# Performance work log

Hardware: AMD Instinct MI355X
Metric: run time of the kernel (lower is better)

Reference implementation:

```python
import jax, jax.numpy as jnp
import numpy as np

G, HQ, D = 8, 4, 64        # kv groups, query heads per group, head size
S, HID = 2048, 2048        # tokens (single prefill sequence), hidden size
SCALE = D ** -0.5


def _rope(x, cos, sin):
    # x: [S, ..., D]; cos/sin: [S, D//2]; GPT-NeoX rotate-half style
    half = D // 2
    shape = (S,) + (1,) * (x.ndim - 2) + (half,)
    c = cos.reshape(shape)
    s = sin.reshape(shape)
    x1, x2 = x[..., :half], x[..., half:]
    return jnp.concatenate([x1 * c - x2 * s, x2 * c + x1 * s], axis=-1)


def setup_inputs() -> dict:
    key = jax.random.key(0)
    k1, k2, k3 = jax.random.split(key, 3)
    hidden_states = jax.random.normal(k1, (S, HID), dtype=jnp.float32)
    w_qkv = jax.random.normal(k2, (HID, G * (HQ + 2) * D), dtype=jnp.float32) * 0.02
    w_dense = jax.random.normal(k3, (HID, HID), dtype=jnp.float32) * 0.02
    inv_freq = 1.0 / (10000.0 ** (jnp.arange(0, D, 2, dtype=jnp.float32) / D))
    freqs = jnp.arange(S, dtype=jnp.float32)[:, None] * inv_freq[None, :]  # [S, D//2]
    return {"hidden_states": hidden_states, "cos": jnp.cos(freqs), "sin": jnp.sin(freqs),
            "w_qkv": w_qkv, "w_dense": w_dense}


def reference(hidden_states, cos, sin, w_qkv, w_dense):
    qkv = hidden_states @ w_qkv                       # [S, G*(HQ+2)*D]
    qkv = qkv.reshape(S, G, HQ + 2, D)
    q = qkv[:, :, :HQ]                                # [S, G, HQ, D]
    k = qkv[:, :, HQ]                                 # [S, G, D]
    v = qkv[:, :, HQ + 1]                             # [S, G, D]
    q = _rope(q, cos, sin)
    k = _rope(k, cos, sin)
    # causal GQA attention (prefill path, single sequence)
    scores = jnp.einsum('sghd,tgd->ghst', q, k) * SCALE   # [G, HQ, S, S]
    causal = jnp.tril(jnp.ones((S, S), dtype=bool))
    scores = jnp.where(causal, scores, jnp.float32(-1e30))
    attn = jax.nn.softmax(scores, axis=-1)
    out = jnp.einsum('ghst,tgd->sghd', attn, v)           # [S, G, HQ, D]
    return out.reshape(S, G * HQ * D) @ w_dense
```

## Files before the change

### kernel.cpp

```cpp
#include <hip/hip_runtime.h>

#define S_LEN 2048
#define HID_DIM 2048
#define NG 8
#define NHQ 4
#define DH 64
#define QSCALE 0.18033688011112042f
#define FIXMAX 12.0f

typedef short short8 __attribute__((ext_vector_type(8)));
typedef float f32x4 __attribute__((ext_vector_type(4)));
typedef unsigned short ushort_t;

__device__ __forceinline__ unsigned short f2bf(float f) {
  unsigned u = __builtin_bit_cast(unsigned, f);
  u += 0x7fffu + ((u >> 16) & 1u);
  return (unsigned short)(u >> 16);
}

__device__ __forceinline__ void mfma16(f32x4& d, short8 a, short8 b) {
  asm volatile("v_mfma_f32_16x16x32_bf16 %0, %1, %2, %0" : "+v"(d) : "v"(a), "v"(b));
}

#define GLDS16(gp, lp) __builtin_amdgcn_global_load_lds( \
    (__attribute__((address_space(1))) void*)(gp),       \
    (__attribute__((address_space(3))) void*)(lp), 16, 0, 0)

__global__ __launch_bounds__(256) void cvt_bf16_k(const float* __restrict__ in,
                                                  ushort_t* __restrict__ out, int n4) {
  int i = blockIdx.x * 256 + threadIdx.x;
  if (i >= n4) return;
  float4 v = ((const float4*)in)[i];
  ushort4 o;
  o.x = f2bf(v.x); o.y = f2bf(v.y); o.z = f2bf(v.z); o.w = f2bf(v.w);
  ((ushort4*)out)[i] = o;
}

__global__ __launch_bounds__(256) void tcvt_k(const float* __restrict__ in,
                                              ushort_t* __restrict__ out, int R, int C) {
  __shared__ ushort_t t[32][33];
  int bx = blockIdx.x * 32, by = blockIdx.y * 32;
  int tx = threadIdx.x & 31, ty = threadIdx.x >> 5;
  for (int j = ty; j < 32; j += 8)
    t[j][tx] = f2bf(in[(long)(by + j) * C + bx + tx]);
  __syncthreads();
  for (int j = ty; j < 32; j += 8)
    out[(long)(bx + j) * R + by + tx] = t[tx][j];
}

__global__ __launch_bounds__(256) void cs_trans_k(const float* __restrict__ cosb,
                                                  const float* __restrict__ sinb,
                                                  float* __restrict__ cosT,
                                                  float* __restrict__ sinT) {
  int idx = blockIdx.x * 256 + threadIdx.x;
  int s = idx >> 5, i = idx & 31;
  cosT[i * 2048 + s] = cosb[s * 32 + i];
  sinT[i * 2048 + s] = sinb[s * 32 + i];
}

#define GEMM_PROLOG()                                                       \
  const int tid = threadIdx.x;                                              \
  const int w = tid >> 6, lane = tid & 63;                                  \
  const int m0 = blockIdx.y * 128, n0 = blockIdx.x * 128;                   \
  const int sl = lane >> 3;                                                 \
  const int sc = (lane & 7) ^ sl;                                           \
  const ushort_t* Ag = A + (size_t)(m0 + 32 * w + sl) * K + sc * 8;         \
  const ushort_t* Bg = BT + (size_t)(n0 + 32 * w + sl) * K + sc * 8;        \
  f32x4 acc[4][4];                                                          \
  _Pragma("unroll") for (int i = 0; i < 4; ++i)                             \
  _Pragma("unroll") for (int j = 0; j < 4; ++j)                             \
      acc[i][j] = (f32x4){0.f, 0.f, 0.f, 0.f};                              \
  const int fr = lane & 15;                                                 \
  const int kq4 = lane >> 4;                                                \
  const int wm = w >> 1, wn = w & 1;

#define GEMM_KLOOP()                                                        \
  for (int kt = 0; kt < K; kt += 64) {                                      \
    GLDS16(Ag,          &Al[(32 * w) * 64]);                                \
    GLDS16(Ag +  8 * K, &Al[(32 * w + 8) * 64]);                            \
    GLDS16(Ag + 16 * K, &Al[(32 * w + 16) * 64]);                           \
    GLDS16(Ag + 24 * K, &Al[(32 * w + 24) * 64]);                           \
    GLDS16(Bg,          &Bl[(32 * w) * 64]);                                \
    GLDS16(Bg +  8 * K, &Bl[(32 * w + 8) * 64]);                            \
    GLDS16(Bg + 16 * K, &Bl[(32 * w + 16) * 64]);                           \
    GLDS16(Bg + 24 * K, &Bl[(32 * w + 24) * 64]);                           \
    Ag += 64; Bg += 64;                                                     \
    __syncthreads();                                                        \
    _Pragma("unroll")                                                       \
    for (int c = 0; c < 2; ++c) {                                           \
      short8 af[4], bfr[4];                                                 \
      _Pragma("unroll") for (int mf = 0; mf < 4; ++mf) {                    \
        const int row = 64 * wm + 16 * mf + fr;                             \
        af[mf] = *(const short8*)&Al[row * 64 +                             \
                 (((kq4 + 4 * c) ^ (row & 7)) << 3)];                       \
      }                                                                     \
      _Pragma("unroll") for (int nf = 0; nf < 4; ++nf) {                    \
        const int row = 64 * wn + 16 * nf + fr;                             \
        bfr[nf] = *(const short8*)&Bl[row * 64 +                            \
                  (((kq4 + 4 * c) ^ (row & 7)) << 3)];                      \
      }                                                                     \
      _Pragma("unroll") for (int mf = 0; mf < 4; ++mf)                      \
      _Pragma("unroll") for (int nf = 0; nf < 4; ++nf)                      \
          mfma16(acc[mf][nf], af[mf], bfr[nf]);                             \
    }                                                                       \
    __syncthreads();                                                        \
  }

__global__ __launch_bounds__(256) void gemm_bt_k(const ushort_t* __restrict__ A,
                                                 const ushort_t* __restrict__ BT,
                                                 float* __restrict__ C,
                                                 int M, int N, int K) {
  __shared__ __align__(16) ushort_t Al[128 * 64];
  __shared__ __align__(16) ushort_t Bl[128 * 64];
  GEMM_PROLOG();
  GEMM_KLOOP();
  const int crow = m0 + 64 * wm + 4 * (lane >> 4);
  const int ccol = n0 + 64 * wn + fr;
#pragma unroll
  for (int mf = 0; mf < 4; ++mf)
#pragma unroll
    for (int nf = 0; nf < 4; ++nf)
#pragma unroll
      for (int r = 0; r < 4; ++r)
        C[(size_t)(crow + 16 * mf + r) * N + ccol + 16 * nf] = acc[mf][nf][r];
}

__global__ __launch_bounds__(256) void gemm_qkv_k(const ushort_t* __restrict__ A,
                                                  const ushort_t* __restrict__ BT,
                                                  const float* __restrict__ cosT,
                                                  const float* __restrict__ sinT,
                                                  ushort_t* __restrict__ Qbf,
                                                  ushort_t* __restrict__ Kbf,
                                                  ushort_t* __restrict__ Vbuf,
                                                  int M, int N, int K) {
  __shared__ __align__(16) ushort_t Al[128 * 64];
  __shared__ __align__(16) ushort_t Bl[128 * 64];
  GEMM_PROLOG();
  GEMM_KLOOP();
  const int crow = m0 + 64 * wm + 4 * (lane >> 4);
  const int hb = ((n0 % 384) >> 6) + wn;
  const int gg = n0 / 384;
  if (hb == 5) {
    ushort_t* dst = Vbuf + (size_t)gg * 2048 * 64;
#pragma unroll
    for (int mf = 0; mf < 4; ++mf)
#pragma unroll
      for (int nf = 0; nf < 4; ++nf)
#pragma unroll
        for (int r = 0; r < 4; ++r)
          dst[(size_t)(crow + 16 * mf + r) * 64 + 16 * nf + fr] =
              f2bf(acc[mf][nf][r]);
  } else {
    const float qs = (hb < 4) ? QSCALE : 1.0f;
    ushort_t* dst = (hb < 4) ? Qbf + (size_t)(gg * 4 + hb) * 2048 * 64
                             : Kbf + (size_t)gg * 2048 * 64;
#pragma unroll
    for (int mf = 0; mf < 4; ++mf) {
#pragma unroll
      for (int nf2 = 0; nf2 < 2; ++nf2) {
        const int i = 16 * nf2 + fr;
        float4 cT = *(const float4*)&cosT[(size_t)i * 2048 + crow + 16 * mf];
        float4 sT = *(const float4*)&sinT[(size_t)i * 2048 + crow + 16 * mf];
        const float cc[4] = {cT.x, cT.y, cT.z, cT.w};
        const float ss[4] = {sT.x, sT.y, sT.z, sT.w};
#pragma unroll
        for (int r = 0; r < 4; ++r) {
          const size_t row = crow + 16 * mf + r;
          float x1 = acc[mf][nf2][r], x2 = acc[mf][nf2 + 2][r];
          dst[row * 64 + i]      = f2bf((x1 * cc[r] - x2 * ss[r]) * qs);
          dst[row * 64 + i + 32] = f2bf((x2 * cc[r] + x1 * ss[r]) * qs);
        }
      }
    }
  }
}

__global__ __launch_bounds__(256) void vtrans_k(const ushort_t* __restrict__ Vbuf,
                                                ushort_t* __restrict__ Vt) {
  __shared__ ushort_t t[64][65];
  int s0 = blockIdx.x * 64, g = blockIdx.y;
  for (int idx = threadIdx.x; idx < 4096; idx += 256) {
    int r = idx >> 6, d = idx & 63;
    t[d][r] = Vbuf[((size_t)g * 2048 + s0 + r) * 64 + d];
  }
  __syncthreads();
  for (int idx = threadIdx.x; idx < 4096; idx += 256) {
    int d = idx >> 6, c = idx & 63;
    Vt[((size_t)g * 64 + d) * 2048 + s0 + c] = t[d][c];
  }
}

__global__ __launch_bounds__(256, 4) void attn9_k(const ushort_t* __restrict__ Qbf,
                                                  const ushort_t* __restrict__ Kbf,
                                                  const ushort_t* __restrict__ Vt,
                                                  ushort_t* __restrict__ outb) {
  __shared__ __align__(16) ushort_t Kl[2][64 * 64];
  __shared__ __align__(16) ushort_t Vl[2][64 * 64];
  __shared__ __align__(16) ushort_t Pl[4][1024];
  const int gh = blockIdx.x;
  const int y = blockIdx.y;
  const int bb = y & 7, aa = y >> 3;
  const int u = (aa == 0) ? 31 - bb : (aa == 1) ? 16 + bb : (aa == 2) ? 15 - bb : bb;
  const int g = gh >> 2;
  const int w = threadIdx.x >> 6, l = threadIdx.x & 63;
  const int li = l & 15, hi = l >> 4;
  const int q0 = 64 * u + 16 * w;
  const int nt = u + 1;

  const ushort_t* Qh = Qbf + (long)gh * 2048 * 64;
  const ushort_t* Kh = Kbf + (long)g * 2048 * 64;
  const ushort_t* Vh = Vt + (long)g * 64 * 2048;
  char* Pw = (char*)&Pl[w][0];

  const int sr = 16 * w + (l >> 3);
  const int sc = (l & 7) ^ (l >> 3);
  const short8 ones = {0x3F80, 0x3F80, 0x3F80, 0x3F80, 0x3F80, 0x3F80, 0x3F80, 0x3F80};

  short8 aq0 = *(const short8*)&Qh[(q0 + li) * 64 + hi * 8];
  short8 aq1 = *(const short8*)&Qh[(q0 + li) * 64 + 32 + hi * 8];

  f32x4 o[4];
#pragma unroll
  for (int df = 0; df < 4; ++df) o[df] = (f32x4){0.f, 0.f, 0.f, 0.f};
  f32x4 os = (f32x4){0.f, 0.f, 0.f, 0.f};

  GLDS16(Kh + (long)sr * 64 + sc * 8,         &Kl[0][(16 * w) * 64]);
  GLDS16(Kh + (long)(sr + 8) * 64 + sc * 8,   &Kl[0][(16 * w + 8) * 64]);
  GLDS16(Vh + (long)sr * 2048 + sc * 8,       &Vl[0][(16 * w) * 64]);
  GLDS16(Vh + (long)(sr + 8) * 2048 + sc * 8, &Vl[0][(16 * w + 8) * 64]);
  __syncthreads();

  int buf = 0;
  for (int it = 0; it < nt; ++it) {
    const int t0 = it * 64;
    if (it + 1 < nt) {
      const int tn = t0 + 64;
      GLDS16(Kh + (long)(tn + sr) * 64 + sc * 8,       &Kl[buf ^ 1][(16 * w) * 64]);
      GLDS16(Kh + (long)(tn + sr + 8) * 64 + sc * 8,   &Kl[buf ^ 1][(16 * w + 8) * 64]);
      GLDS16(Vh + (long)sr * 2048 + tn + sc * 8,       &Vl[buf ^ 1][(16 * w) * 64]);
      GLDS16(Vh + (long)(sr + 8) * 2048 + tn + sc * 8, &Vl[buf ^ 1][(16 * w + 8) * 64]);
    }
    const ushort_t* kb = &Kl[buf][0];
    const ushort_t* vb = &Vl[buf][0];

    f32x4 sf[4];
#pragma unroll
    for (int f = 0; f < 4; ++f) sf[f] = (f32x4){0.f, 0.f, 0.f, 0.f};
    __builtin_amdgcn_s_setprio(1);
#pragma unroll
    for (int f = 0; f < 4; ++f) {
      const int row = 16 * f + li;
      short8 b0 = *(const short8*)&kb[row * 64 + ((hi ^ (row & 7)) << 3)];
      short8 b1 = *(const short8*)&kb[row * 64 + (((hi + 4) ^ (row & 7)) << 3)];
      mfma16(sf[f], aq0, b0);
      mfma16(sf[f], aq1, b1);
    }
    __builtin_amdgcn_s_setprio(0);

    if (t0 + 63 > q0) {
#pragma unroll
      for (int f = 0; f < 4; ++f) {
        int t = t0 + 16 * f + li;
#pragma unroll
        for (int r = 0; r < 4; ++r)
          if (t > q0 + 4 * hi + r) sf[f][r] = -1e30f;
      }
    }
#pragma unroll
    for (int f = 0; f < 4; ++f) {
      int k2 = 2 * (li + 16 * f);
#pragma unroll
      for (int r = 0; r < 4; ++r) {
        float p = __builtin_amdgcn_exp2f(sf[f][r] - FIXMAX);
        int q = 4 * hi + r;
        *(ushort_t*)(Pw + q * 128 + (k2 ^ ((q & 7) << 4))) =
            (ushort_t)(__builtin_bit_cast(unsigned, p) >> 16);
      }
    }

    __builtin_amdgcn_s_setprio(1);
#pragma unroll
    for (int kst = 0; kst < 2; ++kst) {
      short8 pa = *(const short8*)(Pw + li * 128 + (((4 * kst + hi) ^ (li & 7)) << 4));
#pragma unroll
      for (int df = 0; df < 4; ++df) {
        const int row = 16 * df + li;
        short8 bv = *(const short8*)&vb[row * 64 + (((4 * kst + hi) ^ (row & 7)) << 3)];
        mfma16(o[df], pa, bv);
      }
      mfma16(os, pa, ones);
    }
    __builtin_amdgcn_s_setprio(0);

    __syncthreads();
    buf ^= 1;
  }
#pragma unroll
  for (int r = 0; r < 4; ++r) {
    float inv = 1.f / os[r];
#pragma unroll
    for (int df = 0; df < 4; ++df)
      outb[(long)(q0 + 4 * hi + r) * HID_DIM + gh * 64 + 16 * df + li] =
          f2bf(o[df][r] * inv);
  }
}

extern "C" void kernel_launch(void* const* d_in, const int* in_sizes, int n_in,
                              void* d_out, int out_size, void* d_ws, size_t ws_size,
                              hipStream_t stream) {
  const float* X    = (const float*)d_in[0];
  const float* cosb = (const float*)d_in[1];
  const float* sinb = (const float*)d_in[2];
  const float* Wqkv = (const float*)d_in[3];
  const float* Wd   = (const float*)d_in[4];
  float* out = (float*)d_out;

  char* ws = (char*)d_ws;
  ushort_t* Xbf   = (ushort_t*)ws;
  ushort_t* WqkvT = Xbf + (size_t)2048 * 2048;
  ushort_t* WdT   = WqkvT + (size_t)3072 * 2048;
  ushort_t* Qbf   = WdT + (size_t)2048 * 2048;
  ushort_t* Kbf   = Qbf + (size_t)32 * 2048 * 64;
  ushort_t* Vbuf  = Kbf + (size_t)8 * 2048 * 64;
  ushort_t* Vt    = Vbuf + (size_t)8 * 2048 * 64;
  ushort_t* attnO = Vt + (size_t)8 * 2048 * 64;
  float*    cosT  = (float*)(attnO + (size_t)2048 * 2048);
  float*    sinT  = cosT + (size_t)32 * 2048;

  cvt_bf16_k<<<4096, 256, 0, stream>>>(X, Xbf, (2048 * 2048) / 4);
  tcvt_k<<<dim3(3072 / 32, 2048 / 32), 256, 0, stream>>>(Wqkv, WqkvT, 2048, 3072);
  tcvt_k<<<dim3(2048 / 32, 2048 / 32), 256, 0, stream>>>(Wd, WdT, 2048, 2048);
  cs_trans_k<<<256, 256, 0, stream>>>(cosb, sinb, cosT, sinT);

  gemm_qkv_k<<<dim3(3072 / 128, 2048 / 128), 256, 0, stream>>>(
      Xbf, WqkvT, cosT, sinT, Qbf, Kbf, Vbuf, 2048, 3072, 2048);

  vtrans_k<<<dim3(S_LEN / 64, NG), 256, 0, stream>>>(Vbuf, Vt);

  attn9_k<<<dim3(NG * NHQ, 32), 256, 0, stream>>>(Qbf, Kbf, Vt, attnO);

  gemm_bt_k<<<dim3(2048 / 128, 2048 / 128), 256, 0, stream>>>(attnO, WdT, out,
                                                              2048, 2048, 2048);
}
```

Before: 145.2 us.

## Enlarge attention query tile to 128 rows, two 16-row slabs per wave

Each attention block now covers 128 query rows instead of 64, with every wave handling two 16-row query slabs that share each loaded K/V tile. This halves the number of K/V tile loads from global memory per query row and reuses each LDS B-fragment read for two MFMAs. Waves skip compute on tiles that lie entirely above their causal diagonal. The cost is more registers (launch bounds lowered to 2 blocks per SIMD), a larger P buffer in LDS, half as many blocks, and some intra-block imbalance from the skipped tiles.

After: 154.9 us. 1.07x slower.

```diff
diff --git a/kernel.cpp b/kernel.cpp
--- a/kernel.cpp
+++ b/kernel.cpp
@@ -190,118 +190,143 @@
   }
 }
 
-__global__ __launch_bounds__(256, 4) void attn9_k(const ushort_t* __restrict__ Qbf,
-                                                  const ushort_t* __restrict__ Kbf,
-                                                  const ushort_t* __restrict__ Vt,
-                                                  ushort_t* __restrict__ outb) {
+__global__ __launch_bounds__(256, 2) void attn10_k(const ushort_t* __restrict__ Qbf,
+                                                   const ushort_t* __restrict__ Kbf,
+                                                   const ushort_t* __restrict__ Vt,
+                                                   ushort_t* __restrict__ outb) {
   __shared__ __align__(16) ushort_t Kl[2][64 * 64];
   __shared__ __align__(16) ushort_t Vl[2][64 * 64];
-  __shared__ __align__(16) ushort_t Pl[4][1024];
+  __shared__ __align__(16) ushort_t Pl[4][2048];
   const int gh = blockIdx.x;
   const int y = blockIdx.y;
   const int bb = y & 7, aa = y >> 3;
-  const int u = (aa == 0) ? 31 - bb : (aa == 1) ? 16 + bb : (aa == 2) ? 15 - bb : bb;
+  const int u = aa ? bb : 15 - bb;
   const int g = gh >> 2;
   const int w = threadIdx.x >> 6, l = threadIdx.x & 63;
   const int li = l & 15, hi = l >> 4;
-  const int q0 = 64 * u + 16 * w;
-  const int nt = u + 1;
-
-  const ushort_t* Qh = Qbf + (long)gh * 2048 * 64;
-  const ushort_t* Kh = Kbf + (long)g * 2048 * 64;
-  const ushort_t* Vh = Vt + (long)g * 64 * 2048;
+  const int q0 = 128 * u + 32 * w;
+  const int ntb = 2 * u + 2;
+
+  const ushort_t* Qh = Qbf + (size_t)gh * 2048 * 64;
+  const ushort_t* Kh = Kbf + (size_t)g * 2048 * 64;
+  const ushort_t* Vh = Vt + (size_t)g * 64 * 2048;
   char* Pw = (char*)&Pl[w][0];
 
   const int sr = 16 * w + (l >> 3);
   const int sc = (l & 7) ^ (l >> 3);
   const short8 ones = {0x3F80, 0x3F80, 0x3F80, 0x3F80, 0x3F80, 0x3F80, 0x3F80, 0x3F80};
 
-  short8 aq0 = *(const short8*)&Qh[(q0 + li) * 64 + hi * 8];
-  short8 aq1 = *(const short8*)&Qh[(q0 + li) * 64 + 32 + hi * 8];
-
-  f32x4 o[4];
-#pragma unroll
-  for (int df = 0; df < 4; ++df) o[df] = (f32x4){0.f, 0.f, 0.f, 0.f};
-  f32x4 os = (f32x4){0.f, 0.f, 0.f, 0.f};
-
-  GLDS16(Kh + (long)sr * 64 + sc * 8,         &Kl[0][(16 * w) * 64]);
-  GLDS16(Kh + (long)(sr + 8) * 64 + sc * 8,   &Kl[0][(16 * w + 8) * 64]);
-  GLDS16(Vh + (long)sr * 2048 + sc * 8,       &Vl[0][(16 * w) * 64]);
-  GLDS16(Vh + (long)(sr + 8) * 2048 + sc * 8, &Vl[0][(16 * w + 8) * 64]);
+  short8 aq00 = *(const short8*)&Qh[(q0 + li) * 64 + hi * 8];
+  short8 aq01 = *(const short8*)&Qh[(q0 + li) * 64 + 32 + hi * 8];
+  short8 aq10 = *(const short8*)&Qh[(q0 + 16 + li) * 64 + hi * 8];
+  short8 aq11 = *(const short8*)&Qh[(q0 + 16 + li) * 64 + 32 + hi * 8];
+
+  f32x4 o0[4], o1[4];
+#pragma unroll
+  for (int df = 0; df < 4; ++df) {
+    o0[df] = (f32x4){0.f, 0.f, 0.f, 0.f};
+    o1[df] = (f32x4){0.f, 0.f, 0.f, 0.f};
+  }
+  f32x4 os0 = (f32x4){0.f, 0.f, 0.f, 0.f};
+  f32x4 os1 = (f32x4){0.f, 0.f, 0.f, 0.f};
+
+  GLDS16(Kh + (size_t)sr * 64 + sc * 8,         &Kl[0][(16 * w) * 64]);
+  GLDS16(Kh + (size_t)(sr + 8) * 64 + sc * 8,   &Kl[0][(16 * w + 8) * 64]);
+  GLDS16(Vh + (size_t)sr * 2048 + sc * 8,       &Vl[0][(16 * w) * 64]);
+  GLDS16(Vh + (size_t)(sr + 8) * 2048 + sc * 8, &Vl[0][(16 * w + 8) * 64]);
   __syncthreads();
 
   int buf = 0;
-  for (int it = 0; it < nt; ++it) {
+  for (int it = 0; it < ntb; ++it) {
     const int t0 = it * 64;
-    if (it + 1 < nt) {
+    if (it + 1 < ntb) {
       const int tn = t0 + 64;
-      GLDS16(Kh + (long)(tn + sr) * 64 + sc * 8,       &Kl[buf ^ 1][(16 * w) * 64]);
-      GLDS16(Kh + (long)(tn + sr + 8) * 64 + sc * 8,   &Kl[buf ^ 1][(16 * w + 8) * 64]);
-      GLDS16(Vh + (long)sr * 2048 + tn + sc * 8,       &Vl[buf ^ 1][(16 * w) * 64]);
-      GLDS16(Vh + (long)(sr + 8) * 2048 + tn + sc * 8, &Vl[buf ^ 1][(16 * w + 8) * 64]);
+      GLDS16(Kh + (size_t)(tn + sr) * 64 + sc * 8,       &Kl[buf ^ 1][(16 * w) * 64]);
+      GLDS16(Kh + (size_t)(tn + sr + 8) * 64 + sc * 8,   &Kl[buf ^ 1][(16 * w + 8) * 64]);
+      GLDS16(Vh + (size_t)sr * 2048 + tn + sc * 8,       &Vl[buf ^ 1][(16 * w) * 64]);
+      GLDS16(Vh + (size_t)(sr + 8) * 2048 + tn + sc * 8, &Vl[buf ^ 1][(16 * w + 8) * 64]);
     }
-    const ushort_t* kb = &Kl[buf][0];
-    const ushort_t* vb = &Vl[buf][0];
-
-    f32x4 sf[4];
-#pragma unroll
-    for (int f = 0; f < 4; ++f) sf[f] = (f32x4){0.f, 0.f, 0.f, 0.f};
-    __builtin_amdgcn_s_setprio(1);
-#pragma unroll
-    for (int f = 0; f < 4; ++f) {
-      const int row = 16 * f + li;
-      short8 b0 = *(const short8*)&kb[row * 64 + ((hi ^ (row & 7)) << 3)];
-      short8 b1 = *(const short8*)&kb[row * 64 + (((hi + 4) ^ (row & 7)) << 3)];
-      mfma16(sf[f], aq0, b0);
-      mfma16(sf[f], aq1, b1);
+    if (t0 <= q0) {
+      const ushort_t* kb = &Kl[buf][0];
+      const ushort_t* vb = &Vl[buf][0];
+
+      f32x4 sf0[4], sf1[4];
+#pragma unroll
+      for (int f = 0; f < 4; ++f) {
+        sf0[f] = (f32x4){0.f, 0.f, 0.f, 0.f};
+        sf1[f] = (f32x4){0.f, 0.f, 0.f, 0.f};
+      }
+      __builtin_amdgcn_s_setprio(1);
+#pragma unroll
+      for (int f = 0; f < 4; ++f) {
+        const int row = 16 * f + li;
+        short8 b0 = *(const short8*)&kb[row * 64 + ((hi ^ (row & 7)) << 3)];
+        short8 b1 = *(const short8*)&kb[row * 64 + (((hi + 4) ^ (row & 7)) << 3)];
+        mfma16(sf0[f], aq00, b0);
+        mfma16(sf0[f], aq01, b1);
+        mfma16(sf1[f], aq10, b0);
+        mfma16(sf1[f], aq11, b1);
+      }
+      __builtin_amdgcn_s_setprio(0);
+
+      if (t0 + 63 > q0) {
+#pragma unroll
+        for (int f = 0; f < 4; ++f) {
+          int t = t0 + 16 * f + li;
+#pragma unroll
+          for (int r = 0; r < 4; ++r) {
+            if (t > q0 + 4 * hi + r) sf0[f][r] = -1e30f;
+            if (t > q0 + 16 + 4 * hi + r) sf1[f][r] = -1e30f;
+          }
+        }
+      }
+#pragma unroll
+      for (int f = 0; f < 4; ++f) {
+        int k2 = 2 * (li + 16 * f);
+#pragma unroll
+        for (int r = 0; r < 4; ++r) {
+          float p0 = __builtin_amdgcn_exp2f(sf0[f][r] - FIXMAX);
+          float p1 = __builtin_amdgcn_exp2f(sf1[f][r] - FIXMAX);
+          int q = 4 * hi + r;
+          *(ushort_t*)(Pw + q * 128 + (k2 ^ ((q & 7) << 4))) =
+              (ushort_t)(__builtin_bit_cast(unsigned, p0) >> 16);
+          *(ushort_t*)(Pw + (q + 16) * 128 + (k2 ^ ((q & 7) << 4))) =
+              (ushort_t)(__builtin_bit_cast(unsigned, p1) >> 16);
+        }
+      }
+
+      __builtin_amdgcn_s_setprio(1);
+#pragma unroll
+      for (int kst = 0; kst < 2; ++kst) {
+        const int pb = (((4 * kst + hi) ^ (li & 7)) << 4);
+        short8 pa0 = *(const short8*)(Pw + li * 128 + pb);
+        short8 pa1 = *(const short8*)(Pw + (li + 16) * 128 + pb);
+#pragma unroll
+        for (int df = 0; df < 4; ++df) {
+          const int row = 16 * df + li;
+          short8 bv = *(const short8*)&vb[row * 64 + (((4 * kst + hi) ^ (row & 7)) << 3)];
+          mfma16(o0[df], pa0, bv);
+          mfma16(o1[df], pa1, bv);
+        }
+        mfma16(os0, pa0, ones);
+        mfma16(os1, pa1, ones);
+      }
+      __builtin_amdgcn_s_setprio(0);
     }
-    __builtin_amdgcn_s_setprio(0);
-
-    if (t0 + 63 > q0) {
-#pragma unroll
-      for (int f = 0; f < 4; ++f) {
-        int t = t0 + 16 * f + li;
-#pragma unroll
-        for (int r = 0; r < 4; ++r)
-          if (t > q0 + 4 * hi + r) sf[f][r] = -1e30f;
-      }
-    }
-#pragma unroll
-    for (int f = 0; f < 4; ++f) {
-      int k2 = 2 * (li + 16 * f);
-#pragma unroll
-      for (int r = 0; r < 4; ++r) {
-        float p = __builtin_amdgcn_exp2f(sf[f][r] - FIXMAX);
-        int q = 4 * hi + r;
-        *(ushort_t*)(Pw + q * 128 + (k2 ^ ((q & 7) << 4))) =
-            (ushort_t)(__builtin_bit_cast(unsigned, p) >> 16);
-      }
-    }
-
-    __builtin_amdgcn_s_setprio(1);
-#pragma unroll
-    for (int kst = 0; kst < 2; ++kst) {
-      short8 pa = *(const short8*)(Pw + li * 128 + (((4 * kst + hi) ^ (li & 7)) << 4));
-#pragma unroll
-      for (int df = 0; df < 4; ++df) {
-        const int row = 16 * df + li;
-        short8 bv = *(const short8*)&vb[row * 64 + (((4 * kst + hi) ^ (row & 7)) << 3)];
-        mfma16(o[df], pa, bv);
-      }
-      mfma16(os, pa, ones);
-    }
-    __builtin_amdgcn_s_setprio(0);
-
     __syncthreads();
     buf ^= 1;
   }
 #pragma unroll
   for (int r = 0; r < 4; ++r) {
-    float inv = 1.f / os[r];
-#pragma unroll
-    for (int df = 0; df < 4; ++df)
-      outb[(long)(q0 + 4 * hi + r) * HID_DIM + gh * 64 + 16 * df + li] =
-          f2bf(o[df][r] * inv);
+    float inv0 = 1.f / os0[r];
+    float inv1 = 1.f / os1[r];
+#pragma unroll
+    for (int df = 0; df < 4; ++df) {
+      outb[(size_t)(q0 + 4 * hi + r) * HID_DIM + gh * 64 + 16 * df + li] =
+          f2bf(o0[df][r] * inv0);
+      outb[(size_t)(q0 + 16 + 4 * hi + r) * HID_DIM + gh * 64 + 16 * df + li] =
+          f2bf(o1[df][r] * inv1);
+    }
   }
 }
 
@@ -337,7 +362,7 @@
 
   vtrans_k<<<dim3(S_LEN / 64, NG), 256, 0, stream>>>(Vbuf, Vt);
 
-  attn9_k<<<dim3(NG * NHQ, 32), 256, 0, stream>>>(Qbf, Kbf, Vt, attnO);
+  attn10_k<<<dim3(NG * NHQ, 16), 256, 0, stream>>>(Qbf, Kbf, Vt, attnO);
 
   gemm_bt_k<<<dim3(2048 / 128, 2048 / 128), 256, 0, stream>>>(attnO, WdT, out,
                                                               2048, 2048, 2048);
```
